# Kernel optimization log

Hardware: AMD Instinct MI355X
Metric: run time of the kernel (lower is better)

## Reference

```python
import jax, jax.numpy as jnp
import numpy as np

B, N_H, N_W, DIM, HEADS = 2, 64, 64, 768, 12
HINT = 1024
HIDDEN = DIM * 2       # LTRM expand_ratio = 2
K_ECA = 5              # ECA kernel for C=768: int(|log2(768)/2 + 0.5|)=5 (odd)
TH_LO, TH_HI, MIN_EDGE = 0.02, 0.98, 64


def setup_inputs() -> dict:
    key = jax.random.key(0)
    ks = jax.random.split(key, 12)
    N = N_H * N_W
    x = jax.random.normal(ks[0], (B, N, DIM), jnp.float32)
    # alpha hint: left half = uniform noise (uncertain -> edge tokens),
    # right half = binary blocks aligned to the 16px token cells (easy tokens)
    blocks = (jax.random.uniform(ks[1], (B, 1, N_H, N_W)) > 0.5).astype(jnp.float32)
    blocks_up = jnp.repeat(jnp.repeat(blocks, HINT // N_H, axis=2), HINT // N_W, axis=3)
    noise = jax.random.uniform(ks[2], (B, 1, HINT, HINT))
    col = jnp.arange(HINT)[None, None, None, :]
    alpha_hint = jnp.where(col < HINT // 2, noise, blocks_up)
    s = 0.02
    return {
        "x": x,
        "alpha_hint": alpha_hint,
        # global attention (Hiera-style patched MaskUnitAttention, q_stride=1)
        "qkv_w": jax.random.normal(ks[3], (DIM, 3 * DIM), jnp.float32) * s,
        "qkv_b": jnp.zeros((3 * DIM,), jnp.float32),
        "proj_w": jax.random.normal(ks[4], (DIM, DIM), jnp.float32) * s,
        "proj_b": jnp.zeros((DIM,), jnp.float32),
        # LTRM
        "ln_g": jnp.ones((DIM,), jnp.float32),
        "ln_b": jnp.zeros((DIM,), jnp.float32),
        "fc1_w": jax.random.normal(ks[5], (DIM, HIDDEN), jnp.float32) * s,
        "fc1_b": jnp.zeros((HIDDEN,), jnp.float32),
        "fc2_w": jax.random.normal(ks[6], (HIDDEN, DIM), jnp.float32) * s,  # zeros in ckpt; random for non-trivial math
        "fc2_b": jnp.zeros((DIM,), jnp.float32),
        "eca_w": jax.random.normal(ks[7], (K_ECA,), jnp.float32) * 0.2,
    }


def _edge_mask(alpha_hint):
    # F.interpolate(mode='area') with exact integer factor == block mean
    Bn = alpha_hint.shape[0]
    f_h, f_w = HINT // N_H, HINT // N_W
    hint = alpha_hint.reshape(Bn, N_H, f_h, N_W, f_w).mean(axis=(2, 4)).reshape(Bn, N_H * N_W)
    edge = (hint > TH_LO) & (hint < TH_HI)
    # per-batch fallback: too few edge tokens -> route everything to attention
    edge = jnp.where(edge.sum(axis=1, keepdims=True) < MIN_EDGE, True, edge)
    return edge  # [B, N] bool


def _layernorm(h, g, b, eps=1e-5):
    mu = h.mean(-1, keepdims=True)
    var = ((h - mu) ** 2).mean(-1, keepdims=True)
    return (h - mu) * jax.lax.rsqrt(var + eps) * g + b


def reference(x, alpha_hint, qkv_w, qkv_b, proj_w, proj_b,
              ln_g, ln_b, fc1_w, fc1_b, fc2_w, fc2_b, eca_w):
    Bn, N, C = x.shape
    hd = C // HEADS
    edge = _edge_mask(alpha_hint)                      # [B, N] bool

    # ---- edge path: global SDPA restricted to edge tokens (masked form of
    # the gather->attend->scatter routing: same math, edge keys only) ----
    qkv = (x @ qkv_w + qkv_b).reshape(Bn, N, 3, HEADS, hd)
    q = qkv[:, :, 0].transpose(0, 2, 1, 3)             # [B,H,N,hd]
    k = qkv[:, :, 1].transpose(0, 2, 1, 3)
    v = qkv[:, :, 2].transpose(0, 2, 1, 3)
    scores = jnp.einsum('bhqd,bhkd->bhqk', q, k) / jnp.sqrt(jnp.asarray(hd, x.dtype))
    scores = scores + jnp.where(edge[:, None, None, :], 0.0, -1e9).astype(x.dtype)
    attn = jax.nn.softmax(scores, axis=-1)
    o = jnp.einsum('bhqk,bhkd->bhqd', attn, v)
    o = o.transpose(0, 2, 1, 3).reshape(Bn, N, C)
    attn_out = x + (o @ proj_w + proj_b)               # residual around attention

    # ---- easy path: LTRM (subset of tokens -> DWConv branch skipped,
    # exactly as in LTRM.forward when N != H*W) ----
    h = _layernorm(x, ln_g, ln_b)
    h = jax.nn.gelu(h @ fc1_w + fc1_b, approximate=False)
    h = jax.nn.gelu(h, approximate=False)
    h = h @ fc2_w + fc2_b                              # [B,N,C]
    # ECA: avg-pool over the routed (easy) token set -> masked mean
    easy = ~edge
    cnt = jnp.maximum(easy.sum(axis=1).astype(x.dtype), 1.0)      # [B]
    pooled = (h * easy[..., None]).sum(axis=1) / cnt[:, None]     # [B,C]
    g = jax.lax.conv_general_dilated(
        pooled[:, None, :], eca_w.reshape(1, 1, K_ECA), (1,), 'SAME',
        dimension_numbers=('NCH', 'OIH', 'NCH'))[:, 0, :]          # [B,C]
    h = h * jax.nn.sigmoid(g)[:, None, :]
    ltrm_out = x + h

    # ---- scatter-combine ----
    return jnp.where(edge[..., None], attn_out, ltrm_out)
```

## Files before the change

### kernel.cpp

```cpp
#include <hip/hip_runtime.h>

using u16 = unsigned short;
using short8 = __attribute__((ext_vector_type(8))) short;
using f32x4 = __attribute__((ext_vector_type(4))) float;

#define NTOK 4096
#define CDIM 768
#define QKVD 2304
#define NHEAD 12
#define NSPLIT 2
#define SCALE2 0.18033688011112042f

__device__ __forceinline__ u16 f2bf(float f) {
  unsigned u = __float_as_uint(f);
  u += 0x7FFFu + ((u >> 16) & 1u);
  return (u16)(u >> 16);
}
__device__ __forceinline__ float bf2f(u16 v) {
  return __uint_as_float(((unsigned)v) << 16);
}
__device__ __forceinline__ unsigned pkbf(float a, float b) {
  return (unsigned)f2bf(a) | ((unsigned)f2bf(b) << 16);
}

__device__ __forceinline__ void gload_lds16(const void* g, void* l) {
  __builtin_amdgcn_global_load_lds(
      (__attribute__((address_space(1))) void*)g,
      (__attribute__((address_space(3))) void*)l, 16u, 0, 0u);
}

__device__ __forceinline__ float gelu_exact(float z) {
  return 0.5f * z * (1.0f + erff(z * 0.70710678118654752f));
}

__global__ __launch_bounds__(256) void pool_hint_kernel(
    const float* __restrict__ ah, float* __restrict__ hint)
{
  const int bid = blockIdx.x;
  const int b = bid >> 6, cr = bid & 63;
  const int t = threadIdx.x;
  const float* base = ah + ((size_t)b * 1024 + (size_t)cr * 16) * 1024;
  float s = 0.f;
#pragma unroll
  for (int pr = 0; pr < 16; ++pr) {
    float4 v = *(const float4*)(base + (size_t)pr * 1024 + t * 4);
    s += v.x + v.y + v.z + v.w;
  }
  s += __shfl_xor(s, 1);
  s += __shfl_xor(s, 2);
  if ((t & 3) == 0)
    hint[b * NTOK + cr * 64 + (t >> 2)] = s * (1.f / 256.f);
}

__global__ __launch_bounds__(1024) void finalize_edge_kernel(
    const float* __restrict__ hint, int* __restrict__ edge,
    int* __restrict__ qidx, int* __restrict__ eidx,
    int* __restrict__ cntE, int* __restrict__ cntZ)
{
  const int b = blockIdx.x, t = threadIdx.x;
  __shared__ int wsum[16];
  __shared__ int scntE, scntZ, stot;
  int bits[4]; int s = 0;
#pragma unroll
  for (int j = 0; j < 4; ++j) {
    float h = hint[b * NTOK + t * 4 + j];
    bits[j] = (h > 0.02f && h < 0.98f) ? 1 : 0;
    s += bits[j];
    qidx[b * NTOK + t * 4 + j] = -1;
    eidx[b * NTOK + t * 4 + j] = -1;
  }
  int sw = s;
#pragma unroll
  for (int d = 1; d < 64; d <<= 1) sw += __shfl_xor(sw, d);
  const int l = t & 63, w = t >> 6;
  if (l == 0) wsum[w] = sw;
  if (t == 0) { scntE = 0; scntZ = 0; }
  __syncthreads();
  if (t == 0) { int a = 0; for (int i = 0; i < 16; ++i) a += wsum[i]; stot = a; }
  __syncthreads();
  const bool fb = stot < 64;
#pragma unroll
  for (int j = 0; j < 4; ++j) {
    int e = fb ? 1 : bits[j];
    edge[b * NTOK + t * 4 + j] = e;
    if (e) {
      int p = atomicAdd(&scntE, 1);
      qidx[b * NTOK + p] = t * 4 + j;
    } else {
      int p = atomicAdd(&scntZ, 1);
      eidx[b * NTOK + p] = t * 4 + j;
    }
  }
  __syncthreads();
  if (t == 0) { cntE[b] = scntE; cntZ[b] = scntZ; }
}

__global__ __launch_bounds__(256) void ln_kernel(
    const float* __restrict__ x, const float* __restrict__ gam,
    const float* __restrict__ bet, u16* __restrict__ lnb, u16* __restrict__ xb)
{
  const int row = blockIdx.x, t = threadIdx.x;
  const float* xr = x + (size_t)row * CDIM;
  float v[3];
#pragma unroll
  for (int j = 0; j < 3; ++j) v[j] = xr[t + j * 256];
  float s = v[0] + v[1] + v[2];
  float ss = v[0] * v[0] + v[1] * v[1] + v[2] * v[2];
#pragma unroll
  for (int d = 1; d < 64; d <<= 1) { s += __shfl_xor(s, d); ss += __shfl_xor(ss, d); }
  __shared__ float red[8];
  const int l = t & 63, w = t >> 6;
  if (l == 0) { red[w * 2] = s; red[w * 2 + 1] = ss; }
  __syncthreads();
  s = red[0] + red[2] + red[4] + red[6];
  ss = red[1] + red[3] + red[5] + red[7];
  const float mu = s * (1.f / 768.f);
  const float rstd = rsqrtf(ss * (1.f / 768.f) - mu * mu + 1e-5f);
#pragma unroll
  for (int j = 0; j < 3; ++j) {
    const int cc = t + j * 256;
    lnb[(size_t)row * CDIM + cc] = f2bf((v[j] - mu) * rstd * gam[cc] + bet[cc]);
    xb[(size_t)row * CDIM + cc] = f2bf(v[j]);
  }
}

__global__ __launch_bounds__(256) void transpose_all_kernel(
    const float* __restrict__ qkv_w, const float* __restrict__ proj_w,
    const float* __restrict__ fc1_w, const float* __restrict__ fc2_w,
    u16* __restrict__ qkvT, u16* __restrict__ projT,
    u16* __restrict__ fc1T, u16* __restrict__ fc2T)
{
  __shared__ float tile[32][33];
  int bid = blockIdx.x;
  const float* in; u16* outp; int K, N, bx, by;
  if (bid < 1728)      { in = qkv_w;  outp = qkvT; K = 768;  N = 2304; bx = bid % 72; by = bid / 72; }
  else if (bid < 2304) { bid -= 1728; in = proj_w; outp = projT; K = 768;  N = 768;  bx = bid % 24; by = bid / 24; }
  else if (bid < 3456) { bid -= 2304; in = fc1_w;  outp = fc1T; K = 768;  N = 1536; bx = bid % 48; by = bid / 48; }
  else                 { bid -= 3456; in = fc2_w;  outp = fc2T; K = 1536; N = 768;  bx = bid % 24; by = bid / 24; }
  const int tx = threadIdx.x & 31, ty = threadIdx.x >> 5;
#pragma unroll
  for (int j = 0; j < 32; j += 8)
    tile[ty + j][tx] = in[(size_t)(by * 32 + ty + j) * N + bx * 32 + tx];
  __syncthreads();
#pragma unroll
  for (int j = 0; j < 32; j += 8)
    outp[(size_t)(bx * 32 + ty + j) * K + by * 32 + tx] = f2bf(tile[tx][ty + j]);
}

template <int EPI, bool GATHER_A, bool SCATTER_OUT>
__global__ __launch_bounds__(256) void gemm_bt(
    const u16* __restrict__ A, const u16* __restrict__ Bt,
    const float* __restrict__ bias, const float* __restrict__ resid,
    const int* __restrict__ list, void* __restrict__ outp, int N, int K)
{
  const int bm = blockIdx.x, bn = blockIdx.y;
  const int b = bm >> 5, bmi = bm & 31;
  const int rb = bmi * 128;
  if (list[b * NTOK + rb] < 0) return;

  __shared__ __align__(16) u16 lA[128 * 32];
  __shared__ __align__(16) u16 lB[128 * 32];
  const int t = threadIdx.x;
  const int l = t & 63, w = t >> 6;
  const int g = l >> 4, c = l & 15;
  const int wr = w >> 1, wc = w & 1;

  f32x4 acc[4][4];
#pragma unroll
  for (int i = 0; i < 4; ++i)
#pragma unroll
    for (int j = 0; j < 4; ++j) acc[i][j] = f32x4{0.f, 0.f, 0.f, 0.f};

  const int srow = t >> 2;
  const int sslot = (t & 3) ^ (srow & 3);
  int ta0, ta1;
  if constexpr (GATHER_A) {
    ta0 = list[b * NTOK + rb + srow];       if (ta0 < 0) ta0 = 0;
    ta1 = list[b * NTOK + rb + 64 + srow];  if (ta1 < 0) ta1 = 0;
  } else {
    ta0 = rb + srow;
    ta1 = rb + 64 + srow;
  }
  const u16* gA0 = A + ((size_t)b * NTOK + ta0) * K + sslot * 8;
  const u16* gA1 = A + ((size_t)b * NTOK + ta1) * K + sslot * 8;
  const u16* gB0 = Bt + (size_t)(bn * 128 + srow) * K + sslot * 8;
  const u16* gB1 = Bt + (size_t)(bn * 128 + 64 + srow) * K + sslot * 8;
  char* ldA = (char*)lA + w * 1024;
  char* ldB = (char*)lB + w * 1024;

  for (int k0 = 0; k0 < K; k0 += 32) {
    __syncthreads();
    gload_lds16(gA0 + k0, ldA);
    gload_lds16(gA1 + k0, ldA + 4096);
    gload_lds16(gB0 + k0, ldB);
    gload_lds16(gB1 + k0, ldB + 4096);
    __syncthreads();
    short8 af[4], bfr[4];
#pragma unroll
    for (int mi = 0; mi < 4; ++mi) {
      int row = wr * 64 + mi * 16 + c;
      af[mi] = *(const short8*)((const char*)lA + row * 64 + ((g ^ (row & 3)) << 4));
    }
#pragma unroll
    for (int ni = 0; ni < 4; ++ni) {
      int row = wc * 64 + ni * 16 + c;
      bfr[ni] = *(const short8*)((const char*)lB + row * 64 + ((g ^ (row & 3)) << 4));
    }
#pragma unroll
    for (int mi = 0; mi < 4; ++mi)
#pragma unroll
      for (int ni = 0; ni < 4; ++ni)
        acc[mi][ni] = __builtin_amdgcn_mfma_f32_16x16x32_bf16(af[mi], bfr[ni], acc[mi][ni], 0, 0, 0);
  }

#pragma unroll
  for (int mi = 0; mi < 4; ++mi) {
#pragma unroll
    for (int ni = 0; ni < 4; ++ni) {
      const int col = bn * 128 + wc * 64 + ni * 16 + c;
      const float bv = bias[col];
      const int prow0 = rb + wr * 64 + mi * 16 + g * 4;
#pragma unroll
      for (int r = 0; r < 4; ++r) {
        float v = acc[mi][ni][r] + bv;
        int orow;
        if constexpr (SCATTER_OUT) {
          int tok = list[b * NTOK + prow0 + r];
          if (tok < 0) continue;
          orow = tok;
        } else {
          orow = prow0 + r;
        }
        const size_t idx = ((size_t)b * NTOK + orow) * N + col;
        if constexpr (EPI == 0) {
          ((u16*)outp)[idx] = f2bf(v);
        } else if constexpr (EPI == 1) {
          ((float*)outp)[idx] = v + resid[idx];
        } else if constexpr (EPI == 2) {
          ((u16*)outp)[idx] = f2bf(gelu_exact(gelu_exact(v)));
        } else {
          ((float*)outp)[idx] = v;
        }
      }
    }
  }
}

__global__ __launch_bounds__(256) void flash_part_kernel(
    const u16* __restrict__ qkv, const int* __restrict__ cntE,
    u16* __restrict__ partO, float2* __restrict__ partML)
{
  const int qt = blockIdx.x;
  const int bh = blockIdx.y;
  const int sp = blockIdx.z;
  const int b = bh / NHEAD, h = bh % NHEAD;
  const int cnt = cntE[b];
  if (qt * 128 >= cnt) return;

  const int ntiles = (cnt + 63) >> 6;
  const int per = (ntiles + NSPLIT - 1) / NSPLIT;
  const int tA = sp * per;
  const int tB = min(ntiles, tA + per);
  if (tA >= tB) return;

  __shared__ __align__(16) u16 lK[2][64 * 64];
  __shared__ __align__(16) u16 lV[2][64 * 64];
  __shared__ __align__(16) u16 lP[4][32 * 64];

  const int t = threadIdx.x;
  const int l = t & 63, w = t >> 6;
  const int g = l >> 4, c = l & 15;
  const int kp = t & 31, db = t >> 5;
  const size_t tokbase = (size_t)b * NTOK;

  short8 qf[2][2];
#pragma unroll
  for (int mi = 0; mi < 2; ++mi) {
    const int pos = qt * 128 + w * 32 + mi * 16 + c;
    const u16* qp = qkv + (tokbase + pos) * QKVD + h * 64;
#pragma unroll
    for (int kb = 0; kb < 2; ++kb)
      qf[mi][kb] = *(const short8*)(qp + kb * 32 + g * 8);
  }

  f32x4 oacc[2][4];
  float m2run[2], lrun[2];
#pragma unroll
  for (int mi = 0; mi < 2; ++mi) {
#pragma unroll
    for (int nd = 0; nd < 4; ++nd) oacc[mi][nd] = f32x4{0.f, 0.f, 0.f, 0.f};
    m2run[mi] = -1e30f; lrun[mi] = 0.f;
  }

  char* lPw = (char*)lP[w];

  auto stageK = [&](int kt, int buf) {
#pragma unroll
    for (int j = 0; j < 2; ++j) {
      int seg = j * 256 + t;
      int row = seg >> 3;
      int sl = (seg & 7) ^ (row & 7);
      gload_lds16(qkv + (tokbase + kt * 64 + row) * QKVD + CDIM + h * 64 + sl * 8,
                  (char*)lK[buf] + j * 4096 + w * 1024);
    }
  };
  uint4 va, vb;
  auto loadV = [&](int kt) {
    const u16* vg = qkv + (tokbase + kt * 64 + kp * 2) * QKVD + 2 * CDIM + h * 64 + db * 8;
    va = *(const uint4*)vg;
    vb = *(const uint4*)(vg + QKVD);
  };
  auto writeV = [&](int buf) {
    union { uint4 q; u16 s[8]; } u0, u1; u0.q = va; u1.q = vb;
    char* lvb = (char*)lV[buf];
#pragma unroll
    for (int j = 0; j < 8; ++j) {
      int d = db * 8 + j;
      unsigned pk = (unsigned)u0.s[j] | ((unsigned)u1.s[j] << 16);
      *(unsigned*)(lvb + d * 128 + ((kp * 4) ^ ((d & 7) << 4))) = pk;
    }
  };

  int cur = 0;
  stageK(tA, 0);
  loadV(tA);
  writeV(0);
  __syncthreads();

  for (int kt = tA; kt < tB; ++kt) {
    const bool hasNext = (kt + 1 < tB);
    if (hasNext) { stageK(kt + 1, cur ^ 1); loadV(kt + 1); }

    const char* lKc = (const char*)lK[cur];
    short8 kf[4][2];
#pragma unroll
    for (int ni = 0; ni < 4; ++ni) {
      int row = ni * 16 + c;
#pragma unroll
      for (int kb = 0; kb < 2; ++kb)
        kf[ni][kb] = *(const short8*)(lKc + row * 128 + (((kb * 4 + g) ^ (row & 7)) << 4));
    }
    f32x4 st[2][4];
    __builtin_amdgcn_s_setprio(1);
#pragma unroll
    for (int mi = 0; mi < 2; ++mi)
#pragma unroll
      for (int ni = 0; ni < 4; ++ni) {
        f32x4 sv = f32x4{0.f, 0.f, 0.f, 0.f};
        sv = __builtin_amdgcn_mfma_f32_16x16x32_bf16(kf[ni][0], qf[mi][0], sv, 0, 0, 0);
        sv = __builtin_amdgcn_mfma_f32_16x16x32_bf16(kf[ni][1], qf[mi][1], sv, 0, 0, 0);
        st[mi][ni] = sv;
      }
    __builtin_amdgcn_s_setprio(0);

    const int kvalid = cnt - kt * 64;
#pragma unroll
    for (int mi = 0; mi < 2; ++mi)
#pragma unroll
      for (int ni = 0; ni < 4; ++ni)
#pragma unroll
        for (int r = 0; r < 4; ++r) {
          float v = st[mi][ni][r] * SCALE2;
          st[mi][ni][r] = (ni * 16 + g * 4 + r < kvalid) ? v : -1e30f;
        }

#pragma unroll
    for (int mi = 0; mi < 2; ++mi) {
      float mx = fmaxf(
          fmaxf(fmaxf(fmaxf(st[mi][0][0], st[mi][0][1]), fmaxf(st[mi][0][2], st[mi][0][3])),
                fmaxf(fmaxf(st[mi][1][0], st[mi][1][1]), fmaxf(st[mi][1][2], st[mi][1][3]))),
          fmaxf(fmaxf(fmaxf(st[mi][2][0], st[mi][2][1]), fmaxf(st[mi][2][2], st[mi][2][3])),
                fmaxf(fmaxf(st[mi][3][0], st[mi][3][1]), fmaxf(st[mi][3][2], st[mi][3][3]))));
      mx = fmaxf(mx, __shfl_xor(mx, 16));
      mx = fmaxf(mx, __shfl_xor(mx, 32));
      const float m2new = fmaxf(m2run[mi], mx);
      const float alpha = exp2f(m2run[mi] - m2new);
      m2run[mi] = m2new;
      float rs = 0.f;
      const int qrow = mi * 16 + c;
      char* base = lPw + qrow * 128;
      const int swz = (qrow & 7) << 4;
#pragma unroll
      for (int ni = 0; ni < 4; ++ni) {
        float p0 = exp2f(st[mi][ni][0] - m2new);
        float p1 = exp2f(st[mi][ni][1] - m2new);
        float p2 = exp2f(st[mi][ni][2] - m2new);
        float p3 = exp2f(st[mi][ni][3] - m2new);
        rs += (p0 + p1) + (p2 + p3);
        *(uint2*)(base + ((ni * 32 + g * 8) ^ swz)) = make_uint2(pkbf(p0, p1), pkbf(p2, p3));
      }
      rs += __shfl_xor(rs, 16);
      rs += __shfl_xor(rs, 32);
      lrun[mi] = lrun[mi] * alpha + rs;
#pragma unroll
      for (int nd = 0; nd < 4; ++nd)
#pragma unroll
        for (int r = 0; r < 4; ++r) oacc[mi][nd][r] *= alpha;
    }

    const char* lVc = (const char*)lV[cur];
#pragma unroll
    for (int kb = 0; kb < 2; ++kb) {
      short8 pb[2], vf[4];
#pragma unroll
      for (int mi = 0; mi < 2; ++mi) {
        int qrow = mi * 16 + c;
        pb[mi] = *(const short8*)(lPw + qrow * 128 + (((kb * 64 + g * 16)) ^ ((qrow & 7) << 4)));
      }
#pragma unroll
      for (int nd = 0; nd < 4; ++nd) {
        int d = nd * 16 + c;
        vf[nd] = *(const short8*)(lVc + d * 128 + (((kb * 4 + g) ^ (d & 7)) << 4));
      }
      __builtin_amdgcn_s_setprio(1);
#pragma unroll
      for (int mi = 0; mi < 2; ++mi)
#pragma unroll
        for (int nd = 0; nd < 4; ++nd)
          oacc[mi][nd] = __builtin_amdgcn_mfma_f32_16x16x32_bf16(vf[nd], pb[mi], oacc[mi][nd], 0, 0, 0);
      __builtin_amdgcn_s_setprio(0);
    }

    if (hasNext) writeV(cur ^ 1);
    __syncthreads();
    cur ^= 1;
  }

  const size_t pobase = ((size_t)(sp * 2 + b) * NHEAD + h) * NTOK;
#pragma unroll
  for (int mi = 0; mi < 2; ++mi) {
    const int pos = qt * 128 + w * 32 + mi * 16 + c;
    if (pos < cnt) {
      u16* op = partO + (pobase + pos) * 64;
#pragma unroll
      for (int nd = 0; nd < 4; ++nd) {
        ushort4 pk4;
        pk4.x = f2bf(oacc[mi][nd][0]);
        pk4.y = f2bf(oacc[mi][nd][1]);
        pk4.z = f2bf(oacc[mi][nd][2]);
        pk4.w = f2bf(oacc[mi][nd][3]);
        *(ushort4*)(op + nd * 16 + g * 4) = pk4;
      }
      if (g == 0)
        partML[pobase + pos] = make_float2(m2run[mi], lrun[mi]);
    }
  }
}

__global__ __launch_bounds__(256) void flash_merge_kernel(
    const u16* __restrict__ partO, const float2* __restrict__ partML,
    const int* __restrict__ cntE, u16* __restrict__ obf)
{
  const int bh = blockIdx.y;
  const int b = bh / NHEAD, h = bh % NHEAD;
  const int t = threadIdx.x;
  const int pos = blockIdx.x * 4 + (t >> 6);
  const int d = t & 63;
  const int cnt = cntE[b];
  if (pos >= cnt) return;
  const int ntiles = (cnt + 63) >> 6;
  const int per = (ntiles + NSPLIT - 1) / NSPLIT;

  float2 ml[NSPLIT];
  float M = -3e38f;
  int nact = 0;
#pragma unroll
  for (int sp = 0; sp < NSPLIT; ++sp) {
    if (sp * per < ntiles) {
      ml[sp] = partML[((size_t)(sp * 2 + b) * NHEAD + h) * NTOK + pos];
      M = fmaxf(M, ml[sp].x);
      nact = sp + 1;
    }
  }
  float L = 0.f, O = 0.f;
#pragma unroll
  for (int sp = 0; sp < NSPLIT; ++sp) {
    if (sp < nact) {
      const float e = exp2f(ml[sp].x - M);
      L += ml[sp].y * e;
      O += e * bf2f(partO[(((size_t)(sp * 2 + b) * NHEAD + h) * NTOK + pos) * 64 + d]);
    }
  }
  obf[((size_t)b * NTOK + pos) * CDIM + h * 64 + d] = f2bf(O / L);
}

__global__ __launch_bounds__(256) void pool_partial_kernel(
    const float* __restrict__ h2, const int* __restrict__ edge, float* __restrict__ pooled)
{
  const int bid = blockIdx.x;
  const int b = bid / 48, rm = bid % 48;
  const int cg = rm / 16, ts = rm % 16;
  const int ch = cg * 256 + threadIdx.x;
  float s = 0.f;
  for (int tok = ts * 256; tok < ts * 256 + 256; ++tok) {
    if (!edge[b * NTOK + tok])
      s += h2[((size_t)b * NTOK + tok) * CDIM + ch];
  }
  atomicAdd(&pooled[b * CDIM + ch], s);
}

__global__ void eca_kernel(const float* __restrict__ pooled, const float* __restrict__ w5,
                           const int* __restrict__ ecnt, float* __restrict__ gate)
{
  const int b = blockIdx.x, c = threadIdx.x;
  const float inv = 1.f / fmaxf((float)ecnt[b], 1.f);
  float a = 0.f;
#pragma unroll
  for (int j = 0; j < 5; ++j) {
    int i = c - 2 + j;
    if (i >= 0 && i < CDIM) a += w5[j] * pooled[b * CDIM + i];
  }
  a *= inv;
  gate[b * CDIM + c] = 1.f / (1.f + __expf(-a));
}

__global__ __launch_bounds__(256) void combine_kernel(
    const float* __restrict__ x, const float* __restrict__ attn,
    const float* __restrict__ h2, const float* __restrict__ gate,
    const int* __restrict__ edge, float* __restrict__ out)
{
  const size_t i = ((size_t)blockIdx.x * 256 + threadIdx.x) * 4;
  const int b = (int)(i / ((size_t)NTOK * CDIM));
  const size_t r = i % ((size_t)NTOK * CDIM);
  const int tok = (int)(r / CDIM);
  const int cc = (int)(r % CDIM);
  float4 ov;
  if (edge[b * NTOK + tok]) {
    ov = *(const float4*)(attn + i);
  } else {
    float4 xv = *(const float4*)(x + i);
    float4 hv = *(const float4*)(h2 + i);
    float4 gv = *(const float4*)(gate + b * CDIM + cc);
    ov.x = xv.x + hv.x * gv.x;
    ov.y = xv.y + hv.y * gv.y;
    ov.z = xv.z + hv.z * gv.z;
    ov.w = xv.w + hv.w * gv.w;
  }
  *(float4*)(out + i) = ov;
}

extern "C" void kernel_launch(void* const* d_in, const int* in_sizes, int n_in,
                              void* d_out, int out_size, void* d_ws, size_t ws_size,
                              hipStream_t stream) {
  const float* x      = (const float*)d_in[0];
  const float* ah     = (const float*)d_in[1];
  const float* qkv_w  = (const float*)d_in[2];
  const float* qkv_b  = (const float*)d_in[3];
  const float* proj_w = (const float*)d_in[4];
  const float* proj_b = (const float*)d_in[5];
  const float* ln_g   = (const float*)d_in[6];
  const float* ln_b   = (const float*)d_in[7];
  const float* fc1_w  = (const float*)d_in[8];
  const float* fc1_b  = (const float*)d_in[9];
  const float* fc2_w  = (const float*)d_in[10];
  const float* fc2_b  = (const float*)d_in[11];
  const float* eca_w  = (const float*)d_in[12];
  float* out = (float*)d_out;

  char* ws = (char*)d_ws;
  size_t off = 0;
  auto alloc = [&](size_t bytes) {
    char* p = ws + off;
    off += (bytes + 255) & ~(size_t)255;
    return p;
  };
  float* hint   = (float*)alloc((size_t)2 * NTOK * 4);
  int*   edge   = (int*)alloc((size_t)2 * NTOK * 4);
  int*   qidx   = (int*)alloc((size_t)2 * NTOK * 4);
  int*   eidx   = (int*)alloc((size_t)2 * NTOK * 4);
  int*   cntE   = (int*)alloc(256);
  int*   cntZ   = (int*)alloc(256);
  u16*   xbf    = (u16*)alloc((size_t)2 * NTOK * CDIM * 2);
  u16*   lnbf   = (u16*)alloc((size_t)2 * NTOK * CDIM * 2);
  u16*   qkvT   = (u16*)alloc((size_t)QKVD * CDIM * 2);
  u16*   projT  = (u16*)alloc((size_t)CDIM * CDIM * 2);
  u16*   fc1T   = (u16*)alloc((size_t)1536 * CDIM * 2);
  u16*   fc2T   = (u16*)alloc((size_t)CDIM * 1536 * 2);
  u16*   qkvb   = (u16*)alloc((size_t)2 * NTOK * QKVD * 2);
  u16*   obf    = (u16*)alloc((size_t)2 * NTOK * CDIM * 2);
  u16*   h1bf   = (u16*)alloc((size_t)2 * NTOK * 1536 * 2);
  float* h2     = (float*)alloc((size_t)2 * NTOK * CDIM * 4);
  float* attn   = (float*)alloc((size_t)2 * NTOK * CDIM * 4);
  u16*   partO  = (u16*)alloc((size_t)NSPLIT * 2 * NHEAD * NTOK * 64 * 2);
  float* partML = (float*)alloc((size_t)NSPLIT * 2 * NHEAD * NTOK * 8);
  float* pooled = (float*)alloc((size_t)2 * CDIM * 4);
  float* gate   = (float*)alloc((size_t)2 * CDIM * 4);

  pool_hint_kernel<<<dim3(128), 256, 0, stream>>>(ah, hint);
  finalize_edge_kernel<<<dim3(2), 1024, 0, stream>>>(hint, edge, qidx, eidx, cntE, cntZ);
  ln_kernel<<<dim3(8192), 256, 0, stream>>>(x, ln_g, ln_b, lnbf, xbf);
  transpose_all_kernel<<<dim3(4608), 256, 0, stream>>>(
      qkv_w, proj_w, fc1_w, fc2_w, qkvT, projT, fc1T, fc2T);

  gemm_bt<0, true, false><<<dim3(64, 18), 256, 0, stream>>>(
      xbf, qkvT, qkv_b, nullptr, qidx, qkvb, 2304, 768);
  flash_part_kernel<<<dim3(32, 24, NSPLIT), 256, 0, stream>>>(qkvb, cntE, partO, (float2*)partML);
  flash_merge_kernel<<<dim3(1024, 24), 256, 0, stream>>>(partO, (const float2*)partML, cntE, obf);
  gemm_bt<1, false, true><<<dim3(64, 6), 256, 0, stream>>>(
      obf, projT, proj_b, x, qidx, attn, 768, 768);
  gemm_bt<2, true, false><<<dim3(64, 12), 256, 0, stream>>>(
      lnbf, fc1T, fc1_b, nullptr, eidx, h1bf, 1536, 768);
  gemm_bt<3, false, true><<<dim3(64, 6), 256, 0, stream>>>(
      h1bf, fc2T, fc2_b, nullptr, eidx, h2, 768, 1536);

  hipMemsetAsync(pooled, 0, (size_t)2 * CDIM * 4, stream);
  pool_partial_kernel<<<dim3(96), 256, 0, stream>>>(h2, edge, pooled);
  eca_kernel<<<dim3(2), 768, 0, stream>>>(pooled, eca_w, cntZ, gate);
  combine_kernel<<<dim3(6144), 256, 0, stream>>>(x, attn, h2, gate, edge, out);
}
```

Baseline: 530.8 us.

## Rework flash softmax with lazy rescale, raw-exp, split masking, and more KV splits

The flash-attention partial kernel now runs full tiles without masking and handles only the last partial tile with a masked variant. The online softmax folds the scale into an FMA, uses raw v_exp_f32 and hardware packed bf16 conversion, and skips the running-max rescale unless the max grows past a threshold. KV splits rise from 2 to 4 for more parallelism. The partial output buffers now alias the h1bf and attn scratch buffers instead of being separately allocated. This relies on launch ordering so the aliased buffers are not overwritten while still in use, and the lazy rescale allows larger exponent ranges before renormalisation.

```diff
diff --git a/kernel.cpp b/kernel.cpp
--- a/kernel.cpp
+++ b/kernel.cpp
@@ -8,8 +8,9 @@
 #define CDIM 768
 #define QKVD 2304
 #define NHEAD 12
-#define NSPLIT 2
+#define NSPLIT 4
 #define SCALE2 0.18033688011112042f
+#define THRRAW 44.3614195558f
 
 __device__ __forceinline__ u16 f2bf(float f) {
   unsigned u = __float_as_uint(f);
@@ -19,8 +20,15 @@
 __device__ __forceinline__ float bf2f(u16 v) {
   return __uint_as_float(((unsigned)v) << 16);
 }
-__device__ __forceinline__ unsigned pkbf(float a, float b) {
-  return (unsigned)f2bf(a) | ((unsigned)f2bf(b) << 16);
+__device__ __forceinline__ float fast_exp2(float x) {
+  float r;
+  asm("v_exp_f32 %0, %1" : "=v"(r) : "v"(x));
+  return r;
+}
+__device__ __forceinline__ unsigned cvtpk(float lo, float hi) {
+  unsigned r;
+  asm("v_cvt_pk_bf16_f32 %0, %1, %2" : "=v"(r) : "v"(lo), "v"(hi));
+  return r;
 }
 
 __device__ __forceinline__ void gload_lds16(const void* g, void* l) {
@@ -262,6 +270,8 @@
   const int tA = sp * per;
   const int tB = min(ntiles, tA + per);
   if (tA >= tB) return;
+  const int tBf = min(tB, cnt >> 6);
+  const int rem = cnt & 63;
 
   __shared__ __align__(16) u16 lK[2][64 * 64];
   __shared__ __align__(16) u16 lV[2][64 * 64];
@@ -327,104 +337,112 @@
   writeV(0);
   __syncthreads();
 
-  for (int kt = tA; kt < tB; ++kt) {
-    const bool hasNext = (kt + 1 < tB);
-    if (hasNext) { stageK(kt + 1, cur ^ 1); loadV(kt + 1); }
-
-    const char* lKc = (const char*)lK[cur];
-    short8 kf[4][2];
-#pragma unroll
-    for (int ni = 0; ni < 4; ++ni) {
-      int row = ni * 16 + c;
-#pragma unroll
-      for (int kb = 0; kb < 2; ++kb)
-        kf[ni][kb] = *(const short8*)(lKc + row * 128 + (((kb * 4 + g) ^ (row & 7)) << 4));
-    }
-    f32x4 st[2][4];
-    __builtin_amdgcn_s_setprio(1);
-#pragma unroll
-    for (int mi = 0; mi < 2; ++mi)
-#pragma unroll
-      for (int ni = 0; ni < 4; ++ni) {
-        f32x4 sv = f32x4{0.f, 0.f, 0.f, 0.f};
-        sv = __builtin_amdgcn_mfma_f32_16x16x32_bf16(kf[ni][0], qf[mi][0], sv, 0, 0, 0);
-        sv = __builtin_amdgcn_mfma_f32_16x16x32_bf16(kf[ni][1], qf[mi][1], sv, 0, 0, 0);
-        st[mi][ni] = sv;
-      }
-    __builtin_amdgcn_s_setprio(0);
-
-    const int kvalid = cnt - kt * 64;
-#pragma unroll
-    for (int mi = 0; mi < 2; ++mi)
-#pragma unroll
-      for (int ni = 0; ni < 4; ++ni)
-#pragma unroll
-        for (int r = 0; r < 4; ++r) {
-          float v = st[mi][ni][r] * SCALE2;
-          st[mi][ni][r] = (ni * 16 + g * 4 + r < kvalid) ? v : -1e30f;
-        }
-
-#pragma unroll
-    for (int mi = 0; mi < 2; ++mi) {
-      float mx = fmaxf(
-          fmaxf(fmaxf(fmaxf(st[mi][0][0], st[mi][0][1]), fmaxf(st[mi][0][2], st[mi][0][3])),
-                fmaxf(fmaxf(st[mi][1][0], st[mi][1][1]), fmaxf(st[mi][1][2], st[mi][1][3]))),
-          fmaxf(fmaxf(fmaxf(st[mi][2][0], st[mi][2][1]), fmaxf(st[mi][2][2], st[mi][2][3])),
-                fmaxf(fmaxf(st[mi][3][0], st[mi][3][1]), fmaxf(st[mi][3][2], st[mi][3][3]))));
-      mx = fmaxf(mx, __shfl_xor(mx, 16));
-      mx = fmaxf(mx, __shfl_xor(mx, 32));
-      const float m2new = fmaxf(m2run[mi], mx);
-      const float alpha = exp2f(m2run[mi] - m2new);
-      m2run[mi] = m2new;
-      float rs = 0.f;
-      const int qrow = mi * 16 + c;
-      char* base = lPw + qrow * 128;
-      const int swz = (qrow & 7) << 4;
-#pragma unroll
-      for (int ni = 0; ni < 4; ++ni) {
-        float p0 = exp2f(st[mi][ni][0] - m2new);
-        float p1 = exp2f(st[mi][ni][1] - m2new);
-        float p2 = exp2f(st[mi][ni][2] - m2new);
-        float p3 = exp2f(st[mi][ni][3] - m2new);
-        rs += (p0 + p1) + (p2 + p3);
-        *(uint2*)(base + ((ni * 32 + g * 8) ^ swz)) = make_uint2(pkbf(p0, p1), pkbf(p2, p3));
-      }
-      rs += __shfl_xor(rs, 16);
-      rs += __shfl_xor(rs, 32);
-      lrun[mi] = lrun[mi] * alpha + rs;
-#pragma unroll
-      for (int nd = 0; nd < 4; ++nd)
-#pragma unroll
-        for (int r = 0; r < 4; ++r) oacc[mi][nd][r] *= alpha;
-    }
-
-    const char* lVc = (const char*)lV[cur];
-#pragma unroll
-    for (int kb = 0; kb < 2; ++kb) {
-      short8 pb[2], vf[4];
-#pragma unroll
-      for (int mi = 0; mi < 2; ++mi) {
-        int qrow = mi * 16 + c;
-        pb[mi] = *(const short8*)(lPw + qrow * 128 + (((kb * 64 + g * 16)) ^ ((qrow & 7) << 4)));
-      }
-#pragma unroll
-      for (int nd = 0; nd < 4; ++nd) {
-        int d = nd * 16 + c;
-        vf[nd] = *(const short8*)(lVc + d * 128 + (((kb * 4 + g) ^ (d & 7)) << 4));
-      }
-      __builtin_amdgcn_s_setprio(1);
-#pragma unroll
-      for (int mi = 0; mi < 2; ++mi)
-#pragma unroll
-        for (int nd = 0; nd < 4; ++nd)
-          oacc[mi][nd] = __builtin_amdgcn_mfma_f32_16x16x32_bf16(vf[nd], pb[mi], oacc[mi][nd], 0, 0, 0);
-      __builtin_amdgcn_s_setprio(0);
-    }
-
-    if (hasNext) writeV(cur ^ 1);
-    __syncthreads();
-    cur ^= 1;
-  }
+#define FLASH_TILE(MASKED)                                                        \
+  {                                                                               \
+    const bool hasNext = (kt + 1 < tB);                                           \
+    if (hasNext) { stageK(kt + 1, cur ^ 1); loadV(kt + 1); }                      \
+    const char* lKc = (const char*)lK[cur];                                       \
+    short8 kf[4][2];                                                              \
+    _Pragma("unroll")                                                             \
+    for (int ni = 0; ni < 4; ++ni) {                                              \
+      int row = ni * 16 + c;                                                      \
+      _Pragma("unroll")                                                           \
+      for (int kb = 0; kb < 2; ++kb)                                              \
+        kf[ni][kb] = *(const short8*)(lKc + row * 128 +                           \
+                                      (((kb * 4 + g) ^ (row & 7)) << 4));         \
+    }                                                                             \
+    f32x4 st[2][4];                                                               \
+    __builtin_amdgcn_s_setprio(1);                                                \
+    _Pragma("unroll")                                                             \
+    for (int mi = 0; mi < 2; ++mi)                                                \
+      _Pragma("unroll")                                                           \
+      for (int ni = 0; ni < 4; ++ni) {                                            \
+        f32x4 sv = f32x4{0.f, 0.f, 0.f, 0.f};                                     \
+        sv = __builtin_amdgcn_mfma_f32_16x16x32_bf16(kf[ni][0], qf[mi][0], sv, 0, 0, 0); \
+        sv = __builtin_amdgcn_mfma_f32_16x16x32_bf16(kf[ni][1], qf[mi][1], sv, 0, 0, 0); \
+        st[mi][ni] = sv;                                                          \
+      }                                                                           \
+    __builtin_amdgcn_s_setprio(0);                                                \
+    if (MASKED) {                                                                 \
+      _Pragma("unroll")                                                           \
+      for (int mi = 0; mi < 2; ++mi)                                              \
+        _Pragma("unroll")                                                         \
+        for (int ni = 0; ni < 4; ++ni)                                            \
+          _Pragma("unroll")                                                       \
+          for (int r = 0; r < 4; ++r)                                             \
+            if (ni * 16 + g * 4 + r >= rem) st[mi][ni][r] = -1e30f;               \
+    }                                                                             \
+    _Pragma("unroll")                                                             \
+    for (int mi = 0; mi < 2; ++mi) {                                              \
+      float mx = fmaxf(                                                           \
+          fmaxf(fmaxf(fmaxf(st[mi][0][0], st[mi][0][1]), fmaxf(st[mi][0][2], st[mi][0][3])), \
+                fmaxf(fmaxf(st[mi][1][0], st[mi][1][1]), fmaxf(st[mi][1][2], st[mi][1][3]))), \
+          fmaxf(fmaxf(fmaxf(st[mi][2][0], st[mi][2][1]), fmaxf(st[mi][2][2], st[mi][2][3])), \
+                fmaxf(fmaxf(st[mi][3][0], st[mi][3][1]), fmaxf(st[mi][3][2], st[mi][3][3])))); \
+      mx = fmaxf(mx, __shfl_xor(mx, 16));                                         \
+      mx = fmaxf(mx, __shfl_xor(mx, 32));                                         \
+      if (!__all(mx - m2run[mi] <= THRRAW)) {                                     \
+        const float mnew = fmaxf(m2run[mi], mx);                                  \
+        const float alpha = fast_exp2((m2run[mi] - mnew) * SCALE2);               \
+        m2run[mi] = mnew;                                                         \
+        lrun[mi] *= alpha;                                                        \
+        _Pragma("unroll")                                                         \
+        for (int nd = 0; nd < 4; ++nd)                                            \
+          _Pragma("unroll")                                                       \
+          for (int r = 0; r < 4; ++r) oacc[mi][nd][r] *= alpha;                   \
+      }                                                                           \
+      const float msc = m2run[mi] * SCALE2;                                       \
+      float rs = 0.f;                                                             \
+      const int qrow = mi * 16 + c;                                               \
+      char* pbase = lPw + qrow * 128;                                             \
+      const int swz = (qrow & 7) << 4;                                            \
+      _Pragma("unroll")                                                           \
+      for (int ni = 0; ni < 4; ++ni) {                                            \
+        float p0 = fast_exp2(fmaf(st[mi][ni][0], SCALE2, -msc));                  \
+        float p1 = fast_exp2(fmaf(st[mi][ni][1], SCALE2, -msc));                  \
+        float p2 = fast_exp2(fmaf(st[mi][ni][2], SCALE2, -msc));                  \
+        float p3 = fast_exp2(fmaf(st[mi][ni][3], SCALE2, -msc));                  \
+        rs += (p0 + p1) + (p2 + p3);                                              \
+        *(uint2*)(pbase + ((ni * 32 + g * 8) ^ swz)) =                            \
+            make_uint2(cvtpk(p0, p1), cvtpk(p2, p3));                             \
+      }                                                                           \
+      rs += __shfl_xor(rs, 16);                                                   \
+      rs += __shfl_xor(rs, 32);                                                   \
+      lrun[mi] += rs;                                                             \
+    }                                                                             \
+    const char* lVc = (const char*)lV[cur];                                       \
+    _Pragma("unroll")                                                             \
+    for (int kb = 0; kb < 2; ++kb) {                                              \
+      short8 pb[2], vf[4];                                                        \
+      _Pragma("unroll")                                                           \
+      for (int mi = 0; mi < 2; ++mi) {                                            \
+        int qrow = mi * 16 + c;                                                   \
+        pb[mi] = *(const short8*)(lPw + qrow * 128 +                              \
+                                  ((kb * 64 + g * 16) ^ ((qrow & 7) << 4)));      \
+      }                                                                           \
+      _Pragma("unroll")                                                           \
+      for (int nd = 0; nd < 4; ++nd) {                                            \
+        int d = nd * 16 + c;                                                      \
+        vf[nd] = *(const short8*)(lVc + d * 128 +                                 \
+                                  (((kb * 4 + g) ^ (d & 7)) << 4));               \
+      }                                                                           \
+      __builtin_amdgcn_s_setprio(1);                                              \
+      _Pragma("unroll")                                                           \
+      for (int mi = 0; mi < 2; ++mi)                                              \
+        _Pragma("unroll")                                                         \
+        for (int nd = 0; nd < 4; ++nd)                                            \
+          oacc[mi][nd] = __builtin_amdgcn_mfma_f32_16x16x32_bf16(vf[nd], pb[mi], oacc[mi][nd], 0, 0, 0); \
+      __builtin_amdgcn_s_setprio(0);                                              \
+    }                                                                             \
+    if (hasNext) writeV(cur ^ 1);                                                 \
+    __syncthreads();                                                              \
+    cur ^= 1;                                                                     \
+  }
+
+  int kt = tA;
+  for (; kt < tBf; ++kt) FLASH_TILE(0)
+  for (; kt < tB; ++kt) FLASH_TILE(1)
+#undef FLASH_TILE
 
   const size_t pobase = ((size_t)(sp * 2 + b) * NHEAD + h) * NTOK;
 #pragma unroll
@@ -442,7 +460,7 @@
         *(ushort4*)(op + nd * 16 + g * 4) = pk4;
       }
       if (g == 0)
-        partML[pobase + pos] = make_float2(m2run[mi], lrun[mi]);
+        partML[pobase + pos] = make_float2(m2run[mi] * SCALE2, lrun[mi]);
     }
   }
 }
@@ -463,20 +481,18 @@
 
   float2 ml[NSPLIT];
   float M = -3e38f;
-  int nact = 0;
 #pragma unroll
   for (int sp = 0; sp < NSPLIT; ++sp) {
     if (sp * per < ntiles) {
       ml[sp] = partML[((size_t)(sp * 2 + b) * NHEAD + h) * NTOK + pos];
       M = fmaxf(M, ml[sp].x);
-      nact = sp + 1;
     }
   }
   float L = 0.f, O = 0.f;
 #pragma unroll
   for (int sp = 0; sp < NSPLIT; ++sp) {
-    if (sp < nact) {
-      const float e = exp2f(ml[sp].x - M);
+    if (sp * per < ntiles) {
+      const float e = fast_exp2(ml[sp].x - M);
       L += ml[sp].y * e;
       O += e * bf2f(partO[(((size_t)(sp * 2 + b) * NHEAD + h) * NTOK + pos) * 64 + d]);
     }
@@ -581,10 +597,10 @@
   u16*   h1bf   = (u16*)alloc((size_t)2 * NTOK * 1536 * 2);
   float* h2     = (float*)alloc((size_t)2 * NTOK * CDIM * 4);
   float* attn   = (float*)alloc((size_t)2 * NTOK * CDIM * 4);
-  u16*   partO  = (u16*)alloc((size_t)NSPLIT * 2 * NHEAD * NTOK * 64 * 2);
-  float* partML = (float*)alloc((size_t)NSPLIT * 2 * NHEAD * NTOK * 8);
   float* pooled = (float*)alloc((size_t)2 * CDIM * 4);
   float* gate   = (float*)alloc((size_t)2 * CDIM * 4);
+  u16*   partO  = (u16*)h1bf;
+  float* partML = attn;
 
   pool_hint_kernel<<<dim3(128), 256, 0, stream>>>(ah, hint);
   finalize_edge_kernel<<<dim3(2), 1024, 0, stream>>>(hint, edge, qidx, eidx, cntE, cntZ);
```

New measurement: 504.5 us. -5.0%, faster.
